# Kernel optimization log

Measured on AMD Instinct MI355X. Metric: run time of the kernel, lower is better.

The kernel has to match this reference:

```python
import jax, jax.numpy as jnp
import numpy as np
import math

N_HEADS = 16
N_KV_HEADS = 4
D_HEAD = 128
EPS = 1e-6
THETA = 10000.0


def _rmsnorm(x, w):
    var = jnp.mean(x * x, axis=-1, keepdims=True)
    return x * jax.lax.rsqrt(var + EPS) * w


def _rope_tables(S, dtype):
    freqs = 1.0 / THETA ** (jnp.arange(0, D_HEAD, 2, dtype=jnp.float32) / D_HEAD)
    angles = jnp.arange(S, dtype=jnp.float32)[:, None] * freqs[None, :]  # [S, D_HEAD/2]
    angles = jnp.concatenate([angles, angles], axis=-1)  # [S, D_HEAD]
    return jnp.cos(angles).astype(dtype), jnp.sin(angles).astype(dtype)


def _apply_rope(x, cos, sin):
    # x: [B, H, S, D]; rotate-half convention matching cat([angles, angles])
    half = D_HEAD // 2
    x1, x2 = x[..., :half], x[..., half:]
    rot = jnp.concatenate([-x2, x1], axis=-1)
    return x * cos[None, None] + rot * sin[None, None]


def setup_inputs() -> dict:
    key = jax.random.key(0)
    ks = jax.random.split(key, 5)
    B, S, D = 2, 2048, 2048
    s = 0.02
    return {
        "x": jax.random.normal(ks[0], (B, S, D), jnp.float32),
        "Wq": jax.random.normal(ks[1], (D, N_HEADS * D_HEAD), jnp.float32) * s,
        "Wk": jax.random.normal(ks[2], (D, N_KV_HEADS * D_HEAD), jnp.float32) * s,
        "Wv": jax.random.normal(ks[3], (D, N_KV_HEADS * D_HEAD), jnp.float32) * s,
        "Wo": jax.random.normal(ks[4], (D, D), jnp.float32) * s,
        "q_norm_w": jnp.ones((D_HEAD,), jnp.float32),
        "k_norm_w": jnp.ones((D_HEAD,), jnp.float32),
    }


def reference(x, Wq, Wk, Wv, Wo, q_norm_w, k_norm_w):
    B, S, D = x.shape
    groups = N_HEADS // N_KV_HEADS

    q = (x @ Wq).reshape(B, S, N_HEADS, D_HEAD).transpose(0, 2, 1, 3)      # [B,H,S,d]
    k = (x @ Wk).reshape(B, S, N_KV_HEADS, D_HEAD).transpose(0, 2, 1, 3)   # [B,Hkv,S,d]
    v = (x @ Wv).reshape(B, S, N_KV_HEADS, D_HEAD).transpose(0, 2, 1, 3)

    q = _rmsnorm(q, q_norm_w)
    k = _rmsnorm(k, k_norm_w)

    cos, sin = _rope_tables(S, x.dtype)
    q = _apply_rope(q, cos, sin)
    k = _apply_rope(k, cos, sin)

    # GQA broadcast: repeat kv heads into query head dim
    k = jnp.repeat(k, groups, axis=1)  # [B,H,S,d]
    v = jnp.repeat(v, groups, axis=1)

    scale = 1.0 / math.sqrt(D_HEAD)
    scores = jnp.einsum("bhqd,bhkd->bhqk", q, k) * scale
    causal = jnp.tril(jnp.ones((S, S), bool))
    scores = jnp.where(causal[None, None], scores, jnp.finfo(scores.dtype).min)
    probs = jax.nn.softmax(scores, axis=-1)
    out = jnp.einsum("bhqk,bhkd->bhqd", probs, v)  # [B,H,S,d]
    out = out.transpose(0, 2, 1, 3).reshape(B, S, D)
    return out @ Wo
```

## Files before the change

### kernel.cpp

```cpp
#include <hip/hip_runtime.h>
#include <stdint.h>

typedef __attribute__((ext_vector_type(8))) short bf16x8;
typedef __attribute__((ext_vector_type(4))) float f32x4;
typedef __attribute__((ext_vector_type(16))) float f32x16;
typedef unsigned short u16;
typedef unsigned int   u32;
typedef unsigned long long u64;

#define S_LEN 2048
#define NH    16
#define NKV   4
#define DH    128
#define DM    2048
#define QKV_N 3072
#define MROWS 4096

__device__ __forceinline__ u16 f2bf(float x) {
  u32 u = __float_as_uint(x);
  return (u16)((u + 0x7fffu + ((u >> 16) & 1u)) >> 16);
}
__device__ __forceinline__ float bf2f(u16 h) {
  return __uint_as_float(((u32)h) << 16);
}
__device__ __forceinline__ u32 cvtpk(float lo, float hi) {
  u32 r;
  asm("v_cvt_pk_bf16_f32 %0, %1, %2" : "=v"(r) : "v"(lo), "v"(hi));
  return r;
}
__device__ __forceinline__ void plswap(u32& a, u32& b) {
  asm volatile("v_permlane32_swap_b32 %0, %1" : "+v"(a), "+v"(b));
}
__device__ __forceinline__ void gload_lds16(const void* g, void* l) {
  __builtin_amdgcn_global_load_lds((const __attribute__((address_space(1))) void*)g,
                                   (__attribute__((address_space(3))) void*)l, 16, 0, 0);
}

__global__ void __launch_bounds__(256) convert_x_kernel(const float* __restrict__ x,
                                                        u16* __restrict__ o) {
  int idx = (blockIdx.x * 256 + threadIdx.x) * 8;
  float4 a = *(const float4*)(x + idx);
  float4 b = *(const float4*)(x + idx + 4);
  union { u16 s[8]; uint4 v; } t;
  t.s[0] = f2bf(a.x); t.s[1] = f2bf(a.y); t.s[2] = f2bf(a.z); t.s[3] = f2bf(a.w);
  t.s[4] = f2bf(b.x); t.s[5] = f2bf(b.y); t.s[6] = f2bf(b.z); t.s[7] = f2bf(b.w);
  *(uint4*)(o + idx) = t.v;
}

__global__ void __launch_bounds__(256) transpose_all_kernel(const float* __restrict__ Wq,
                                                            const float* __restrict__ Wk,
                                                            const float* __restrict__ Wv,
                                                            const float* __restrict__ Wo,
                                                            u16* __restrict__ wqkvt,
                                                            u16* __restrict__ wot) {
  const int z = blockIdx.z;
  const float* src = (z == 0) ? Wq : (z == 1) ? Wk : (z == 2) ? Wv : Wo;
  u16* dst = (z == 0) ? wqkvt
           : (z == 1) ? (wqkvt + (size_t)2048 * 2048)
           : (z == 2) ? (wqkvt + (size_t)2560 * 2048)
           : wot;
  const int N = (z == 1 || z == 2) ? 512 : 2048;
  if (blockIdx.y * 64 >= N) return;
  __shared__ float t[64][65];
  const int bx = blockIdx.x, by = blockIdx.y, tid = threadIdx.x;
#pragma unroll
  for (int rep = 0; rep < 16; ++rep) {
    int lin = rep * 256 + tid;
    int i = lin >> 6, jj = lin & 63;
    t[i][jj] = src[(size_t)(bx * 64 + i) * N + by * 64 + jj];
  }
  __syncthreads();
#pragma unroll
  for (int rep = 0; rep < 16; ++rep) {
    int lin = rep * 256 + tid;
    int nr = lin >> 6, kc = lin & 63;
    dst[(size_t)(by * 64 + nr) * DM + bx * 64 + kc] = f2bf(t[kc][nr]);
  }
}

__global__ void __launch_bounds__(256) rope_tables_kernel(float* __restrict__ ct,
                                                          float* __restrict__ st_) {
  int idx = blockIdx.x * 256 + threadIdx.x;
  int s = idx >> 6, i = idx & 63;
  const float L2_10000 = 13.287712379549449f;
  float freq = exp2f(-(float)i * (1.0f / 64.0f) * L2_10000);
  float ang = (float)s * freq;
  ct[idx] = cosf(ang);
  st_[idx] = sinf(ang);
}

template <int OUTF32>
__global__ void __launch_bounds__(256) gemm_bt(const u16* __restrict__ A,
                                               const u16* __restrict__ Bt,
                                               void* __restrict__ C,
                                               int M, int N, int K) {
  __shared__ __align__(16) u16 As[128 * 32];
  __shared__ __align__(16) u16 Bs[128 * 32];
  const int tid = threadIdx.x;
  const int w = tid >> 6, l = tid & 63;
  const int g = l >> 4, q15 = l & 15;

  const int nwg = gridDim.x * gridDim.y;
  int bid = blockIdx.y * gridDim.x + blockIdx.x;
  {
    int q = nwg >> 3, r = nwg & 7;
    int xcd = bid & 7, idx = bid >> 3;
    bid = (xcd < r ? xcd * (q + 1) : r * (q + 1) + (xcd - r) * q) + idx;
  }
  const int bx = bid % gridDim.x, by = bid / gridDim.x;
  const int row0 = by * 128, col0 = bx * 128;
  const int wm = (w >> 1) * 64, wn = (w & 1) * 64;
  const f32x4 fz = {0.f, 0.f, 0.f, 0.f};
  f32x4 acc[4][4];
#pragma unroll
  for (int m = 0; m < 4; ++m)
#pragma unroll
    for (int n = 0; n < 4; ++n) acc[m][n] = fz;

  for (int kt = 0; kt < K; kt += 32) {
#pragma unroll
    for (int c = 0; c < 2; ++c) {
      int P = (w * 2 + c) * 1024;
      int Pl = P + l * 16;
      int arow = Pl >> 6, acolb = Pl & 63;
      gload_lds16((const char*)A + ((size_t)(row0 + arow) * K + kt) * 2 + acolb,
                  (char*)As + P);
      gload_lds16((const char*)Bt + ((size_t)(col0 + arow) * K + kt) * 2 + acolb,
                  (char*)Bs + P);
    }
    __syncthreads();
    bf16x8 af[4], bfv[4];
#pragma unroll
    for (int m = 0; m < 4; ++m)
      af[m] = *(const bf16x8*)((const char*)As + (wm + m * 16 + q15) * 64 + g * 16);
#pragma unroll
    for (int n = 0; n < 4; ++n)
      bfv[n] = *(const bf16x8*)((const char*)Bs + (wn + n * 16 + q15) * 64 + g * 16);
#pragma unroll
    for (int m = 0; m < 4; ++m)
#pragma unroll
      for (int n = 0; n < 4; ++n)
        acc[m][n] = __builtin_amdgcn_mfma_f32_16x16x32_bf16(af[m], bfv[n], acc[m][n], 0, 0, 0);
    __syncthreads();
  }
#pragma unroll
  for (int m = 0; m < 4; ++m)
#pragma unroll
    for (int n = 0; n < 4; ++n)
#pragma unroll
      for (int r = 0; r < 4; ++r) {
        int rr = row0 + wm + m * 16 + g * 4 + r;
        int cc = col0 + wn + n * 16 + q15;
        float v = acc[m][n][r];
        if (OUTF32) ((float*)C)[(size_t)rr * N + cc] = v;
        else        ((u16*)C)[(size_t)rr * N + cc]  = f2bf(v);
      }
}

__global__ void __launch_bounds__(256) norm_rope_kernel(const u16* __restrict__ qkv,
                                                        const float* __restrict__ qw,
                                                        const float* __restrict__ kw,
                                                        const float* __restrict__ ct,
                                                        const float* __restrict__ st_,
                                                        u16* __restrict__ Qo,
                                                        u16* __restrict__ Ko) {
  int wid = blockIdx.x * 4 + (threadIdx.x >> 6);
  int l = threadIdx.x & 63;
  int row = wid / 20;
  int j = wid - row * 20;
  int b = row >> 11, s = row & 2047;
  bool isq = j < 16;
  int h = isq ? j : (j - 16);
  const u16* src = qkv + (size_t)row * QKV_N + (isq ? h * DH : (2048 + h * DH));
  float x1 = bf2f(src[l]), x2 = bf2f(src[l + 64]);
  float ss = x1 * x1 + x2 * x2;
#pragma unroll
  for (int off = 32; off > 0; off >>= 1) ss += __shfl_xor(ss, off);
  float rn = rsqrtf(ss * (1.0f / 128.0f) + 1e-6f);
  const float* wv = isq ? qw : kw;
  float n1 = x1 * rn * wv[l], n2 = x2 * rn * wv[l + 64];
  float cv = ct[s * 64 + l], sv = st_[s * 64 + l];
  float o1 = n1 * cv - n2 * sv;
  float o2 = n2 * cv + n1 * sv;
  float scale = isq ? 0.08838834764831845f : 1.0f;
  u16* dst = isq ? (Qo + ((size_t)(b * NH + h) * S_LEN + s) * DH)
                 : (Ko + ((size_t)(b * NKV + h) * S_LEN + s) * DH);
  dst[l]      = f2bf(o1 * scale);
  dst[l + 64] = f2bf(o2 * scale);
}

__global__ void __launch_bounds__(256) vtrans_kernel(const u16* __restrict__ qkv,
                                                     u16* __restrict__ vt) {
  __shared__ u16 t[64][65];
  const int st = blockIdx.x, dt = blockIdx.y, bz = blockIdx.z;
  const int tid = threadIdx.x;
#pragma unroll
  for (int rep = 0; rep < 16; ++rep) {
    int lin = rep * 256 + tid;
    int i = lin >> 6, jj = lin & 63;
    t[i][jj] = qkv[(size_t)((bz >> 2) * S_LEN + st * 64 + i) * QKV_N
                   + 2560 + (bz & 3) * DH + dt * 64 + jj];
  }
  __syncthreads();
#pragma unroll
  for (int rep = 0; rep < 16; ++rep) {
    int lin = rep * 256 + tid;
    int dr = lin >> 6, sc = lin & 63;
    vt[((size_t)bz * DH + dt * 64 + dr) * S_LEN + st * 64 + sc] = t[sc][dr];
  }
}

__global__ void __launch_bounds__(256, 2) attn_kernel(const u16* __restrict__ Qg,
                                                      const u16* __restrict__ Kg,
                                                      const u16* __restrict__ Vt,
                                                      u16* __restrict__ O) {
  __shared__ __align__(16) char smem[65536];
  const int tid = threadIdx.x;
  const int w = tid >> 6, l = tid & 63;
  const int q31 = l & 31, hi = l >> 5;
  const int id = blockIdx.x;
  const int grp = id & 7;
  const int mem = (id >> 3) & 3;
  const int tq  = 15 - (id >> 5);
  const int b   = grp >> 2, kvh = grp & 3;
  const int h   = kvh * 4 + mem;
  const int qb  = tq * 128;
  const int nkt = 2 * tq + 1;
  const int qg  = qb + w * 32 + q31;

  bf16x8 qreg[8];
  const u16* Qrow = Qg + ((size_t)(b * NH + h) * S_LEN + qg) * DH;
#pragma unroll
  for (int c = 0; c < 8; ++c)
    qreg[c] = *(const bf16x8*)(Qrow + c * 16 + hi * 8);

  const char* Kbase = (const char*)(Kg + (size_t)(b * NKV + kvh) * S_LEN * DH);
  const char* Vbase = (const char*)(Vt + (size_t)(b * NKV + kvh) * DH * S_LEN);

  auto stage = [&](int buf, int kt) {
    char* Ksb = smem + buf * 32768;
    char* Vsb = Ksb + 16384;
    const char* Kt  = Kbase + (size_t)kt * 64 * 256;
    const char* Vtb = Vbase + (size_t)kt * 128;
#pragma unroll
    for (int i = 0; i < 4; ++i) {
      int off = w * 4096 + i * 1024 + l * 16;
      int row = off >> 8;
      {
        int cb = (off & 255) ^ ((row & 15) << 4);
        gload_lds16(Kt + (size_t)row * 256 + cb, Ksb + off); }
      {
        int qoff = (off & 255) ^ ((row & 15) << 4);
        int d = row * 2 + (qoff >> 7);
        int kvb = qoff & 127;
        gload_lds16(Vtb + (size_t)d * (S_LEN * 2) + kvb, Vsb + off); }
    }
  };

  f32x16 acc[4];
#pragma unroll
  for (int dt = 0; dt < 4; ++dt)
#pragma unroll
    for (int r = 0; r < 16; ++r) acc[dt][r] = 0.f;
  float mrun = -1e30f, lrun = 0.f;

  stage(0, 0);
  __syncthreads();
  int cur = 0;

  for (int kt = 0; kt <= nkt; ++kt) {
    if (kt < nkt) stage(cur ^ 1, kt + 1);
    const char* Ks = smem + cur * 32768;
    const char* Vs = Ks + 16384;

    f32x16 sa[2];
#pragma unroll
    for (int s = 0; s < 2; ++s)
#pragma unroll
      for (int r = 0; r < 16; ++r) sa[s][r] = 0.f;
    __builtin_amdgcn_s_setprio(1);
#pragma unroll
    for (int s = 0; s < 2; ++s) {
      int krow = s * 32 + q31;
      const char* kr = Ks + krow * 256;
      int sw = (krow & 15) << 4;
#pragma unroll
      for (int c = 0; c < 8; ++c) {
        bf16x8 kf = *(const bf16x8*)(kr + ((c * 32 + hi * 16) ^ sw));
        sa[s] = __builtin_amdgcn_mfma_f32_32x32x16_bf16(kf, qreg[c], sa[s], 0, 0, 0);
      }
    }
    __builtin_amdgcn_s_setprio(0);

    const bool domask = (kt * 64 + 63) > (qb + w * 32);
    float tmax = -1e30f;
#pragma unroll
    for (int s = 0; s < 2; ++s)
#pragma unroll
      for (int r = 0; r < 16; ++r) {
        float v = sa[s][r];
        if (domask) {
          int kvg = kt * 64 + s * 32 + (r & 3) + 8 * (r >> 2) + 4 * hi;
          if (kvg > qg) v = -1e30f;
        }
        sa[s][r] = v;
        tmax = fmaxf(tmax, v);
      }
    tmax = fmaxf(tmax, __shfl_xor(tmax, 32));

    const bool defer = __all(tmax <= mrun + 8.0f);
    const float mnew = defer ? mrun : fmaxf(mrun, tmax);

    float tsum = 0.f;
    union { u32 u[4]; bf16x8 v; } pf[4];
#pragma unroll
    for (int s = 0; s < 2; ++s)
#pragma unroll
      for (int kl = 0; kl < 2; ++kl) {
        float e0 = __expf(sa[s][kl * 8 + 0] - mnew);
        float e1 = __expf(sa[s][kl * 8 + 1] - mnew);
        float e2 = __expf(sa[s][kl * 8 + 2] - mnew);
        float e3 = __expf(sa[s][kl * 8 + 3] - mnew);
        float e4 = __expf(sa[s][kl * 8 + 4] - mnew);
        float e5 = __expf(sa[s][kl * 8 + 5] - mnew);
        float e6 = __expf(sa[s][kl * 8 + 6] - mnew);
        float e7 = __expf(sa[s][kl * 8 + 7] - mnew);
        tsum += (e0 + e1) + (e2 + e3) + (e4 + e5) + (e6 + e7);
        u32 A0 = cvtpk(e0, e1), A1 = cvtpk(e2, e3);
        u32 B0 = cvtpk(e4, e5), B1 = cvtpk(e6, e7);
        plswap(A0, B0);
        plswap(A1, B1);
        int ks = s * 2 + kl;
        pf[ks].u[0] = A0; pf[ks].u[1] = A1; pf[ks].u[2] = B0; pf[ks].u[3] = B1;
      }
    tsum += __shfl_xor(tsum, 32);

    if (defer) {
      lrun += tsum;
    } else {
      float alpha = __expf(mrun - mnew);
      lrun = lrun * alpha + tsum;
      mrun = mnew;
#pragma unroll
      for (int dt = 0; dt < 4; ++dt)
#pragma unroll
        for (int r = 0; r < 16; ++r) acc[dt][r] *= alpha;
    }

    __builtin_amdgcn_s_setprio(1);
#pragma unroll
    for (int dt = 0; dt < 4; ++dt) {
      int d = dt * 32 + q31;
      int vrow = d >> 1;
      const char* vr = Vs + vrow * 256;
      int sw = (vrow & 15) << 4;
      int hb = (d & 1) << 7;
#pragma unroll
      for (int ks = 0; ks < 4; ++ks) {
        bf16x8 vf = *(const bf16x8*)(vr + ((hb | (ks * 32 + hi * 16)) ^ sw));
        acc[dt] = __builtin_amdgcn_mfma_f32_32x32x16_bf16(vf, pf[ks].v, acc[dt], 0, 0, 0);
      }
    }
    __builtin_amdgcn_s_setprio(0);

    __syncthreads();
    cur ^= 1;
  }

  const float linv = 1.0f / lrun;
  u16* Obase = O + ((size_t)b * S_LEN + qg) * DM + h * DH;
#pragma unroll
  for (int dt = 0; dt < 4; ++dt)
#pragma unroll
    for (int rg = 0; rg < 4; ++rg) {
      int d0 = dt * 32 + rg * 8 + hi * 4;
      u32 w0 = cvtpk(acc[dt][rg * 4 + 0] * linv, acc[dt][rg * 4 + 1] * linv);
      u32 w1 = cvtpk(acc[dt][rg * 4 + 2] * linv, acc[dt][rg * 4 + 3] * linv);
      u64 vv = (u64)w0 | ((u64)w1 << 32);
      *(u64*)(Obase + d0) = vv;
    }
}

extern "C" void kernel_launch(void* const* d_in, const int* in_sizes, int n_in,
                              void* d_out, int out_size, void* d_ws, size_t ws_size,
                              hipStream_t stream) {
  (void)in_sizes; (void)n_in; (void)out_size; (void)ws_size;
  const float* x  = (const float*)d_in[0];
  const float* Wq = (const float*)d_in[1];
  const float* Wk = (const float*)d_in[2];
  const float* Wv = (const float*)d_in[3];
  const float* Wo = (const float*)d_in[4];
  const float* qw = (const float*)d_in[5];
  const float* kw = (const float*)d_in[6];

  char* ws = (char*)d_ws;
  u16*   xb    = (u16*)(ws + 0);
  u16*   wqkvt = (u16*)(ws + 16777216);
  u16*   wot   = (u16*)(ws + 29360128);
  u16*   qo    = (u16*)(ws + 37748736);
  u16*   ko    = (u16*)(ws + 54525952);
  u16*   vt    = (u16*)(ws + 58720256);
  float* ctab  = (float*)(ws + 62914560);
  float* stab  = (float*)(ws + 63438848);
  u16*   qkvp  = (u16*)d_out;
  u16*   attn  = (u16*)(ws + 0);
  float* outp  = (float*)d_out;

  convert_x_kernel<<<4096, 256, 0, stream>>>(x, xb);
  transpose_all_kernel<<<dim3(32, 32, 4), 256, 0, stream>>>(Wq, Wk, Wv, Wo, wqkvt, wot);
  rope_tables_kernel<<<512, 256, 0, stream>>>(ctab, stab);

  gemm_bt<0><<<dim3(24, 32), 256, 0, stream>>>(xb, wqkvt, qkvp, MROWS, QKV_N, DM);
  norm_rope_kernel<<<20480, 256, 0, stream>>>(qkvp, qw, kw, ctab, stab, qo, ko);
  vtrans_kernel<<<dim3(32, 2, 8), 256, 0, stream>>>(qkvp, vt);
  attn_kernel<<<512, 256, 0, stream>>>(qo, ko, vt, attn);
  gemm_bt<1><<<dim3(16, 32), 256, 0, stream>>>(attn, wot, outp, MROWS, DM, DM);
}
```

Before: 230.9 us.

## Double GEMM K-tile to 64 and XOR-swizzle LDS layout

The bf16 GEMM now stages 64-wide K slices of A and B into LDS instead of 32, which halves the number of loop iterations and barrier pairs per output tile. Each row is stored with a 16-byte XOR swizzle keyed on the row index, and the same swizzle is applied on global load and on LDS read, so the fragment reads for the MFMA inputs avoid bank conflicts. LDS use per block doubles, which may reduce occupancy, and loads are still not overlapped with compute.

```diff
diff --git a/kernel.cpp b/kernel.cpp
--- a/kernel.cpp
+++ b/kernel.cpp
@@ -94,8 +94,8 @@
                                                const u16* __restrict__ Bt,
                                                void* __restrict__ C,
                                                int M, int N, int K) {
-  __shared__ __align__(16) u16 As[128 * 32];
-  __shared__ __align__(16) u16 Bs[128 * 32];
+  __shared__ __align__(16) u16 As[128 * 64];
+  __shared__ __align__(16) u16 Bs[128 * 64];
   const int tid = threadIdx.x;
   const int w = tid >> 6, l = tid & 63;
   const int g = l >> 4, q15 = l & 15;
@@ -117,30 +117,39 @@
 #pragma unroll
     for (int n = 0; n < 4; ++n) acc[m][n] = fz;
 
-  for (int kt = 0; kt < K; kt += 32) {
-#pragma unroll
-    for (int c = 0; c < 2; ++c) {
-      int P = (w * 2 + c) * 1024;
-      int Pl = P + l * 16;
-      int arow = Pl >> 6, acolb = Pl & 63;
-      gload_lds16((const char*)A + ((size_t)(row0 + arow) * K + kt) * 2 + acolb,
-                  (char*)As + P);
-      gload_lds16((const char*)Bt + ((size_t)(col0 + arow) * K + kt) * 2 + acolb,
-                  (char*)Bs + P);
+  for (int kt = 0; kt < K; kt += 64) {
+#pragma unroll
+    for (int rnd = 0; rnd < 4; ++rnd) {
+      int Pl = rnd * 4096 + tid * 16;
+      int arow = Pl >> 7, off = Pl & 127;
+      int scol = off ^ ((arow & 7) << 4);
+      gload_lds16((const char*)A + ((size_t)(row0 + arow) * K + kt) * 2 + scol,
+                  (char*)As + Pl);
+      gload_lds16((const char*)Bt + ((size_t)(col0 + arow) * K + kt) * 2 + scol,
+                  (char*)Bs + Pl);
     }
     __syncthreads();
-    bf16x8 af[4], bfv[4];
-#pragma unroll
-    for (int m = 0; m < 4; ++m)
-      af[m] = *(const bf16x8*)((const char*)As + (wm + m * 16 + q15) * 64 + g * 16);
-#pragma unroll
-    for (int n = 0; n < 4; ++n)
-      bfv[n] = *(const bf16x8*)((const char*)Bs + (wn + n * 16 + q15) * 64 + g * 16);
-#pragma unroll
-    for (int m = 0; m < 4; ++m)
-#pragma unroll
-      for (int n = 0; n < 4; ++n)
-        acc[m][n] = __builtin_amdgcn_mfma_f32_16x16x32_bf16(af[m], bfv[n], acc[m][n], 0, 0, 0);
+#pragma unroll
+    for (int kk = 0; kk < 2; ++kk) {
+      bf16x8 af[4], bfv[4];
+#pragma unroll
+      for (int m = 0; m < 4; ++m) {
+        int row = wm + m * 16 + q15;
+        af[m] = *(const bf16x8*)((const char*)As + row * 128
+                                 + ((kk * 64 + g * 16) ^ ((row & 7) << 4)));
+      }
+#pragma unroll
+      for (int n = 0; n < 4; ++n) {
+        int row = wn + n * 16 + q15;
+        bfv[n] = *(const bf16x8*)((const char*)Bs + row * 128
+                                  + ((kk * 64 + g * 16) ^ ((row & 7) << 4)));
+      }
+#pragma unroll
+      for (int m = 0; m < 4; ++m)
+#pragma unroll
+        for (int n = 0; n < 4; ++n)
+          acc[m][n] = __builtin_amdgcn_mfma_f32_16x16x32_bf16(af[m], bfv[n], acc[m][n], 0, 0, 0);
+    }
     __syncthreads();
   }
 #pragma unroll
```

Measured after the change: 207.1 us (median of 2 runs). -10.3%, faster.
